# Optimization experiments

Hardware: AMD Instinct MI355X
Metric: run time of the kernel (lower is better)

Reference implementation:

```python
import jax, jax.numpy as jnp
import numpy as np

N_WINDOW = 5
FEATS = 512
N_HIDDEN = 16
N = N_WINDOW * FEATS  # 2560


def leaky(x, slope):
    return jnp.where(x >= 0, x, slope * x)


def setup_inputs() -> dict:
    key = jax.random.key(0)
    ks = jax.random.split(key, 16)
    s = 0.05
    return {
        "data": jax.random.normal(ks[0], (1, N_WINDOW, FEATS), jnp.float32),
        "W1": jax.random.normal(ks[1], (N_HIDDEN, N), jnp.float32) * s,
        "b1": jax.random.normal(ks[2], (N_HIDDEN,), jnp.float32) * s,
        "W2": jax.random.normal(ks[3], (N_HIDDEN, N_HIDDEN), jnp.float32) * s,
        "b2": jax.random.normal(ks[4], (N_HIDDEN,), jnp.float32) * s,
        "W3": jax.random.normal(ks[5], (N_WINDOW, N_HIDDEN), jnp.float32) * s,
        "b3": jax.random.normal(ks[6], (N_WINDOW,), jnp.float32) * s,
        "gat_w": jax.random.normal(ks[7], (FEATS,), jnp.float32) * s,
        "a_src": jax.random.normal(ks[8], (FEATS,), jnp.float32) * s,
        "a_dst": jax.random.normal(ks[9], (FEATS,), jnp.float32) * s,
        "gat_bias": jax.random.normal(ks[10], (FEATS,), jnp.float32) * s,
        "F1": jax.random.normal(ks[11], (N_HIDDEN, FEATS), jnp.float32) * s,
        "fb1": jax.random.normal(ks[12], (N_HIDDEN,), jnp.float32) * s,
        "F2": jax.random.normal(ks[13], (N_WINDOW, N_HIDDEN), jnp.float32) * s,
        "fb2": jax.random.normal(ks[14], (N_WINDOW,), jnp.float32) * s,
    }


def reference(data, W1, b1, W2, b2, W3, b3, gat_w, a_src, a_dst, gat_bias, F1, fb1, F2, fb2):
    # ---- attention MLP: Flatten -> Linear -> LeakyReLU(1.0) -> Linear -> LeakyReLU(1.0) -> Linear -> Softmax(dim=0)
    flat = data.reshape(data.shape[0], -1)          # (1, n)
    h = leaky(flat @ W1.T + b1, 1.0)                 # slope True==1.0 -> identity (faithful)
    h = leaky(h @ W2.T + b2, 1.0)
    scores = h @ W3.T + b3                           # (1, n_window)
    att = jax.nn.softmax(scores, axis=0)             # softmax over batch dim (size 1 -> ones)
    att = att.reshape(-1, N_WINDOW, 1)               # (1, 5, 1)

    # ---- weighted window reduction: data_r = data^T @ att
    d = data.reshape(-1, N_WINDOW, FEATS)            # (1, 5, feats)
    data_r = jnp.matmul(jnp.swapaxes(d, -1, -2), att)  # (1, feats, 1)
    x = data_r.reshape(FEATS)                        # node features, scalar per node

    # ---- GATConv(in=1, out=1, heads=feats) on complete graph (self loops included)
    xW = x[:, None] * gat_w[None, :]                 # (N, H): per-head linear transform
    e_src = xW * a_src[None, :]                      # (N, H)
    e_dst = xW * a_dst[None, :]                      # (N, H)
    # logits e[i, j, h] for dst i, src j, head h
    e = leaky(e_dst[:, None, :] + e_src[None, :, :], 0.2)   # (N, N, H)
    alpha = jax.nn.softmax(e, axis=1)                # softmax over source nodes j
    feat_r = jnp.einsum('ijh,jh->ih', alpha, xW) + gat_bias  # (feats, feats)

    # ---- fcn: Linear -> LeakyReLU(1.0) -> Linear -> Sigmoid
    y = leaky(feat_r @ F1.T + fb1, 1.0)
    y = jax.nn.sigmoid(y @ F2.T + fb2)               # (feats, 5)
    return y.reshape(-1)
```

## Files before the change

kernel.cpp:

```cpp
#include <hip/hip_runtime.h>
#include <hip/hip_bf16.h>

#define FEATS 512
#define NW 5
#define NH 16
#define NOUT 5

#define MOFF 1024
#define GOFF (MOFF + 8 * 513)
#define COFF (GOFF + NOUT * FEATS)
#define WS_FLOATS_NEEDED (COFF + NOUT)

template <int CTRL, int RMASK>
__device__ __forceinline__ float dpp_addf(float v) {
    const int r = __builtin_amdgcn_update_dpp(0, __float_as_int(v), CTRL, RMASK, 0xf, true);
    return v + __int_as_float(r);
}
__device__ __forceinline__ float scan64(float v) {
    v = dpp_addf<0x111, 0xf>(v);
    v = dpp_addf<0x112, 0xf>(v);
    v = dpp_addf<0x114, 0xf>(v);
    v = dpp_addf<0x118, 0xf>(v);
    v = dpp_addf<0x142, 0xa>(v);
    v = dpp_addf<0x143, 0xc>(v);
    return v;
}
template <int CTRL, int RMASK>
__device__ __forceinline__ int dpp_addi(int v) {
    const int r = __builtin_amdgcn_update_dpp(0, v, CTRL, RMASK, 0xf, true);
    return v + r;
}
__device__ __forceinline__ int scan64i(int v) {
    v = dpp_addi<0x111, 0xf>(v);
    v = dpp_addi<0x112, 0xf>(v);
    v = dpp_addi<0x114, 0xf>(v);
    v = dpp_addi<0x118, 0xf>(v);
    v = dpp_addi<0x142, 0xa>(v);
    v = dpp_addi<0x143, 0xc>(v);
    return v;
}

__global__ __launch_bounds__(512) void prep_sort(const float* __restrict__ data,
                                                 float* __restrict__ ws) {
    __shared__ float xs[FEATS];
    const int t = threadIdx.x;
    float v = 0.f;
    #pragma unroll
    for (int w = 0; w < NW; ++w) v += data[w * FEATS + t];
    xs[t] = v;
    __syncthreads();

    const int wid = t >> 6, lane = t & 63;
    const int i = blockIdx.x * 8 + wid;
    const float vi = xs[i];
    int r = 0;
    #pragma unroll
    for (int u = 0; u < 8; ++u) {
        const int j = u * 64 + lane;
        const float xj = xs[j];
        r += (xj < vi) || (xj == vi && j < i);
    }
    r = scan64i(r);
    if (lane == 63) ws[FEATS + r] = vi;
    if (blockIdx.x == 0) ws[t] = xs[t];
}

__global__ __launch_bounds__(512) void moments(const float* __restrict__ F1,
                                               const float* __restrict__ fb1,
                                               const float* __restrict__ F2,
                                               const float* __restrict__ fb2,
                                               float* __restrict__ ws) {
    __shared__ float wt[8][8];
    const int t = threadIdx.x, lane = t & 63, wid = t >> 6;

    const float u = ws[FEATS + t];
    const float u2 = u * u,  u3 = u2 * u, u4 = u3 * u;
    const float u5 = u4 * u, u6 = u5 * u, u7 = u6 * u, u8 = u7 * u;

    float s1 = scan64(u),  s2 = scan64(u2), s3 = scan64(u3), s4 = scan64(u4);
    float s5 = scan64(u5), s6 = scan64(u6), s7 = scan64(u7), s8 = scan64(u8);
    if (lane == 63) {
        wt[0][wid] = s1; wt[1][wid] = s2; wt[2][wid] = s3; wt[3][wid] = s4;
        wt[4][wid] = s5; wt[5][wid] = s6; wt[6][wid] = s7; wt[7][wid] = s8;
    }
    __syncthreads();
    float o1 = 0, o2 = 0, o3 = 0, o4 = 0, o5 = 0, o6 = 0, o7 = 0, o8 = 0;
    #pragma unroll
    for (int w = 0; w < 7; ++w) {
        if (w < wid) {
            o1 += wt[0][w]; o2 += wt[1][w]; o3 += wt[2][w]; o4 += wt[3][w];
            o5 += wt[4][w]; o6 += wt[5][w]; o7 += wt[6][w]; o8 += wt[7][w];
        }
    }
    ws[MOFF + 0 * 513 + t + 1] = s1 + o1;  ws[MOFF + 1 * 513 + t + 1] = s2 + o2;
    ws[MOFF + 2 * 513 + t + 1] = s3 + o3;  ws[MOFF + 3 * 513 + t + 1] = s4 + o4;
    ws[MOFF + 4 * 513 + t + 1] = s5 + o5;  ws[MOFF + 5 * 513 + t + 1] = s6 + o6;
    ws[MOFF + 6 * 513 + t + 1] = s7 + o7;  ws[MOFF + 7 * 513 + t + 1] = s8 + o8;
    if (t == 0) {
        #pragma unroll
        for (int p = 0; p < 8; ++p) ws[MOFF + p * 513] = 0.f;
    }

    #pragma unroll
    for (int o = 0; o < NOUT; ++o) {
        float g = 0.f;
        #pragma unroll
        for (int k = 0; k < NH; ++k) g = fmaf(F2[o * NH + k], F1[k * FEATS + t], g);
        ws[GOFF + o * FEATS + t] = g;
    }
    if (t < NOUT) {
        float c = fb2[t];
        #pragma unroll
        for (int k = 0; k < NH; ++k) c = fmaf(F2[t * NH + k], fb1[k], c);
        ws[COFF + t] = c;
    }
}

__global__ __launch_bounds__(512) void gat_out(
    const float* __restrict__ ws,
    const float* __restrict__ gat_w, const float* __restrict__ a_src,
    const float* __restrict__ a_dst, const float* __restrict__ gat_bias,
    float* __restrict__ out)
{
    __shared__ float xsrt[FEATS];
    __shared__ float Mt[8 * 513];
    __shared__ float part[NOUT][8];

    const int t = threadIdx.x, lane = t & 63, wid = t >> 6;
    const int i = blockIdx.x;
    const float LOG2E = 1.4426950408889634f;

    xsrt[t] = ws[FEATS + t];
    #pragma unroll
    for (int q = 0; q < 8; ++q) Mt[q * 512 + t] = ws[MOFF + q * 512 + t];
    if (t < 8) Mt[4096 + t] = ws[MOFF + 4096 + t];

    const float xi   = ws[i];
    const float gw   = gat_w[t];
    const float asr  = a_src[t];
    const float ads  = a_dst[t];
    const float bias = gat_bias[t];
    float Gv[NOUT];
    #pragma unroll
    for (int o = 0; o < NOUT; ++o) Gv[o] = ws[GOFF + o * FEATS + t];
    __syncthreads();

    const float a  = gw * asr;
    const float d  = gw * ads * xi;
    const float a2 = 0.2f * a;
    const bool csn = (a >= 0.f);

    int m = 0;
    #pragma unroll
    for (int step = 256; step; step >>= 1) {
        const int cand = m + step;
        const float tt = fmaf(xsrt[cand - 1], a, d);
        const bool p = csn ? (tt >= 0.f) : (tt < 0.f);
        if (!p) m = cand;
    }

    float P[8], N[8];
    #pragma unroll
    for (int p = 0; p < 8; ++p) {
        const float Pp = Mt[p * 513 + m];
        const float Tp = Mt[p * 513 + 512];
        P[p] = Pp; N[p] = Tp - Pp;
    }
    const float P0 = (float)m, N0 = (float)(FEATS - m);

    float Fv_[8], Qv_[8];
    #pragma unroll
    for (int p = 0; p < 8; ++p) { Fv_[p] = csn ? N[p] : P[p]; Qv_[p] = csn ? P[p] : N[p]; }
    const float F0 = csn ? N0 : P0;
    const float Q0 = csn ? P0 : N0;

    const float r2 = 0.5f, r3 = 1.f/6.f, r4 = 1.f/24.f, r5 = 1.f/120.f,
                r6 = 1.f/720.f, r7 = 1.f/5040.f;
    float h;
    h = Fv_[6] * r7; h = fmaf(h, a, Fv_[5] * r6); h = fmaf(h, a, Fv_[4] * r5);
    h = fmaf(h, a, Fv_[3] * r4); h = fmaf(h, a, Fv_[2] * r3); h = fmaf(h, a, Fv_[1] * r2);
    h = fmaf(h, a, Fv_[0]);
    const float Fe = fmaf(h, a, F0);
    h = Fv_[7] * r7; h = fmaf(h, a, Fv_[6] * r6); h = fmaf(h, a, Fv_[5] * r5);
    h = fmaf(h, a, Fv_[4] * r4); h = fmaf(h, a, Fv_[3] * r3); h = fmaf(h, a, Fv_[2] * r2);
    h = fmaf(h, a, Fv_[1]);
    const float Fw = fmaf(h, a, Fv_[0]);
    h = Qv_[6] * r7; h = fmaf(h, a2, Qv_[5] * r6); h = fmaf(h, a2, Qv_[4] * r5);
    h = fmaf(h, a2, Qv_[3] * r4); h = fmaf(h, a2, Qv_[2] * r3); h = fmaf(h, a2, Qv_[1] * r2);
    h = fmaf(h, a2, Qv_[0]);
    const float Pe = fmaf(h, a2, Q0);
    h = Qv_[7] * r7; h = fmaf(h, a2, Qv_[6] * r6); h = fmaf(h, a2, Qv_[5] * r5);
    h = fmaf(h, a2, Qv_[4] * r4); h = fmaf(h, a2, Qv_[3] * r3); h = fmaf(h, a2, Qv_[2] * r2);
    h = fmaf(h, a2, Qv_[1]);
    const float Pw = fmaf(h, a2, Qv_[0]);

    const float A1 = __builtin_amdgcn_exp2f(LOG2E * d);
    const float A2 = __builtin_amdgcn_exp2f(0.2f * LOG2E * d);
    const float Se = A1 * Fe + A2 * Pe;
    const float Sv = A1 * Fw + A2 * Pw;
    const float feat = gw * (Sv / Se) + bias;

    #pragma unroll
    for (int o = 0; o < NOUT; ++o) {
        const float p = scan64(feat * Gv[o]);
        if (lane == 63) part[o][wid] = p;
    }
    __syncthreads();
    if (t < NOUT) {
        float s = ws[COFF + t];
        #pragma unroll
        for (int w = 0; w < 8; ++w) s += part[t][w];
        out[i * NOUT + t] = 1.f / (1.f + __builtin_amdgcn_exp2f(-s * LOG2E));
    }
}

__global__ __launch_bounds__(512) void gat_fused_fb(
    const float* __restrict__ data,
    const float* __restrict__ gat_w, const float* __restrict__ a_src,
    const float* __restrict__ a_dst, const float* __restrict__ gat_bias,
    const float* __restrict__ F1, const float* __restrict__ fb1,
    const float* __restrict__ F2, const float* __restrict__ fb2,
    float* __restrict__ out)
{
    __shared__ __align__(16) float xs[FEATS];
    __shared__ float feat[FEATS];
    __shared__ float part[NH][8];
    __shared__ float hv[NH];
    const int h = threadIdx.x;
    const int i = blockIdx.x;
    float v = 0.f;
    #pragma unroll
    for (int w = 0; w < NW; ++w) v += data[w * FEATS + h];
    xs[h] = v;
    __syncthreads();
    const float LOG2E = 1.4426950408889634f;
    const float gwv = gat_w[h];
    const float cs = gwv * a_src[h] * LOG2E;
    const float cd = gwv * a_dst[h] * LOG2E;
    const float di = xs[i] * cd;
    float se = 0.f, sv = 0.f;
    const float4* x4 = (const float4*)xs;
    for (int j4 = 0; j4 < FEATS / 4; ++j4) {
        float4 q = x4[j4];
        #pragma unroll
        for (int u = 0; u < 4; ++u) {
            float xj = (u == 0) ? q.x : (u == 1) ? q.y : (u == 2) ? q.z : q.w;
            float tt = fmaf(xj, cs, di);
            float l  = fmaxf(tt, 0.2f * tt);
            float e  = __builtin_amdgcn_exp2f(l);
            se += e;
            sv = fmaf(e, xj, sv);
        }
    }
    feat[h] = gwv * sv / se + gat_bias[h];
    __syncthreads();
    const int lane = h & 63, wid = h >> 6;
    const float fv = feat[h];
    for (int k = 0; k < NH; ++k) {
        float p = fv * F1[k * FEATS + h];
        #pragma unroll
        for (int off = 32; off; off >>= 1) p += __shfl_xor(p, off);
        if (lane == 0) part[k][wid] = p;
    }
    __syncthreads();
    if (h < NH) {
        float s = fb1[h];
        #pragma unroll
        for (int w = 0; w < 8; ++w) s += part[h][w];
        hv[h] = s;
    }
    __syncthreads();
    if (h < 5) {
        float s = fb2[h];
        #pragma unroll
        for (int k = 0; k < NH; ++k) s = fmaf(hv[k], F2[h * NH + k], s);
        out[i * 5 + h] = 1.f / (1.f + __builtin_amdgcn_exp2f(-s * LOG2E));
    }
}

extern "C" void kernel_launch(void* const* d_in, const int* in_sizes, int n_in,
                              void* d_out, int out_size, void* d_ws, size_t ws_size,
                              hipStream_t stream) {
    (void)in_sizes; (void)n_in; (void)out_size;
    const float* data     = (const float*)d_in[0];
    const float* gat_w    = (const float*)d_in[7];
    const float* a_src    = (const float*)d_in[8];
    const float* a_dst    = (const float*)d_in[9];
    const float* gat_bias = (const float*)d_in[10];
    const float* F1       = (const float*)d_in[11];
    const float* fb1      = (const float*)d_in[12];
    const float* F2       = (const float*)d_in[13];
    const float* fb2      = (const float*)d_in[14];
    float* out = (float*)d_out;

    if (ws_size >= (size_t)WS_FLOATS_NEEDED * sizeof(float)) {
        float* ws = (float*)d_ws;
        prep_sort<<<64, FEATS, 0, stream>>>(data, ws);
        moments<<<1, FEATS, 0, stream>>>(F1, fb1, F2, fb2, ws);
        gat_out<<<FEATS, FEATS, 0, stream>>>(ws, gat_w, a_src, a_dst, gat_bias, out);
    } else {
        gat_fused_fb<<<FEATS, FEATS, 0, stream>>>(data, gat_w, a_src, a_dst, gat_bias,
                                                  F1, fb1, F2, fb2, out);
    }
}
```

Baseline: 17.52 us.

## Fuse moments kernel into GAT output kernel, recomputing prefix moments per block

Removes the single-block moments kernel and folds its work into the per-row GAT kernel. Each of the 512 blocks now recomputes the power prefix sums of the sorted features, the F2·F1 projection and the bias constant itself, and reads x_i directly from the input data. This drops one kernel launch and a serial single-block stage plus the workspace round trip, in exchange for redundant per-block computation and extra global reads of F1.

```diff
diff --git a/kernel.cpp b/kernel.cpp
--- a/kernel.cpp
+++ b/kernel.cpp
@@ -6,10 +6,7 @@
 #define NH 16
 #define NOUT 5
 
-#define MOFF 1024
-#define GOFF (MOFF + 8 * 513)
-#define COFF (GOFF + NOUT * FEATS)
-#define WS_FLOATS_NEEDED (COFF + NOUT)
+#define WS_FLOATS_NEEDED FEATS
 
 template <int CTRL, int RMASK>
 __device__ __forceinline__ float dpp_addf(float v) {
@@ -61,28 +58,54 @@
         r += (xj < vi) || (xj == vi && j < i);
     }
     r = scan64i(r);
-    if (lane == 63) ws[FEATS + r] = vi;
-    if (blockIdx.x == 0) ws[t] = xs[t];
-}
-
-__global__ __launch_bounds__(512) void moments(const float* __restrict__ F1,
-                                               const float* __restrict__ fb1,
-                                               const float* __restrict__ F2,
-                                               const float* __restrict__ fb2,
-                                               float* __restrict__ ws) {
+    if (lane == 63) ws[r] = vi;
+}
+
+__global__ __launch_bounds__(512) void gat_all(
+    const float* __restrict__ ws, const float* __restrict__ data,
+    const float* __restrict__ gat_w, const float* __restrict__ a_src,
+    const float* __restrict__ a_dst, const float* __restrict__ gat_bias,
+    const float* __restrict__ F1, const float* __restrict__ fb1,
+    const float* __restrict__ F2, const float* __restrict__ fb2,
+    float* __restrict__ out)
+{
+    __shared__ float xsrt[FEATS];
+    __shared__ float Mt[8 * 513];
     __shared__ float wt[8][8];
+    __shared__ float part[NOUT][8];
+
     const int t = threadIdx.x, lane = t & 63, wid = t >> 6;
-
-    const float u = ws[FEATS + t];
+    const int i = blockIdx.x;
+    const float LOG2E = 1.4426950408889634f;
+
+    const float u = ws[t];
+    xsrt[t] = u;
+
     const float u2 = u * u,  u3 = u2 * u, u4 = u3 * u;
     const float u5 = u4 * u, u6 = u5 * u, u7 = u6 * u, u8 = u7 * u;
-
     float s1 = scan64(u),  s2 = scan64(u2), s3 = scan64(u3), s4 = scan64(u4);
     float s5 = scan64(u5), s6 = scan64(u6), s7 = scan64(u7), s8 = scan64(u8);
     if (lane == 63) {
         wt[0][wid] = s1; wt[1][wid] = s2; wt[2][wid] = s3; wt[3][wid] = s4;
         wt[4][wid] = s5; wt[5][wid] = s6; wt[6][wid] = s7; wt[7][wid] = s8;
     }
+
+    const float gw   = gat_w[t];
+    const float asr  = a_src[t];
+    const float ads  = a_dst[t];
+    const float bias = gat_bias[t];
+    float Gv[NOUT];
+    #pragma unroll
+    for (int o = 0; o < NOUT; ++o) {
+        float g = 0.f;
+        #pragma unroll
+        for (int k = 0; k < NH; ++k) g = fmaf(F2[o * NH + k], F1[k * FEATS + t], g);
+        Gv[o] = g;
+    }
+    float xi = 0.f;
+    #pragma unroll
+    for (int w = 0; w < NW; ++w) xi += data[w * FEATS + i];
+
     __syncthreads();
     float o1 = 0, o2 = 0, o3 = 0, o4 = 0, o5 = 0, o6 = 0, o7 = 0, o8 = 0;
     #pragma unroll
@@ -92,57 +115,14 @@
             o5 += wt[4][w]; o6 += wt[5][w]; o7 += wt[6][w]; o8 += wt[7][w];
         }
     }
-    ws[MOFF + 0 * 513 + t + 1] = s1 + o1;  ws[MOFF + 1 * 513 + t + 1] = s2 + o2;
-    ws[MOFF + 2 * 513 + t + 1] = s3 + o3;  ws[MOFF + 3 * 513 + t + 1] = s4 + o4;
-    ws[MOFF + 4 * 513 + t + 1] = s5 + o5;  ws[MOFF + 5 * 513 + t + 1] = s6 + o6;
-    ws[MOFF + 6 * 513 + t + 1] = s7 + o7;  ws[MOFF + 7 * 513 + t + 1] = s8 + o8;
+    Mt[0 * 513 + t + 1] = s1 + o1;  Mt[1 * 513 + t + 1] = s2 + o2;
+    Mt[2 * 513 + t + 1] = s3 + o3;  Mt[3 * 513 + t + 1] = s4 + o4;
+    Mt[4 * 513 + t + 1] = s5 + o5;  Mt[5 * 513 + t + 1] = s6 + o6;
+    Mt[6 * 513 + t + 1] = s7 + o7;  Mt[7 * 513 + t + 1] = s8 + o8;
     if (t == 0) {
         #pragma unroll
-        for (int p = 0; p < 8; ++p) ws[MOFF + p * 513] = 0.f;
-    }
-
-    #pragma unroll
-    for (int o = 0; o < NOUT; ++o) {
-        float g = 0.f;
-        #pragma unroll
-        for (int k = 0; k < NH; ++k) g = fmaf(F2[o * NH + k], F1[k * FEATS + t], g);
-        ws[GOFF + o * FEATS + t] = g;
-    }
-    if (t < NOUT) {
-        float c = fb2[t];
-        #pragma unroll
-        for (int k = 0; k < NH; ++k) c = fmaf(F2[t * NH + k], fb1[k], c);
-        ws[COFF + t] = c;
-    }
-}
-
-__global__ __launch_bounds__(512) void gat_out(
-    const float* __restrict__ ws,
-    const float* __restrict__ gat_w, const float* __restrict__ a_src,
-    const float* __restrict__ a_dst, const float* __restrict__ gat_bias,
-    float* __restrict__ out)
-{
-    __shared__ float xsrt[FEATS];
-    __shared__ float Mt[8 * 513];
-    __shared__ float part[NOUT][8];
-
-    const int t = threadIdx.x, lane = t & 63, wid = t >> 6;
-    const int i = blockIdx.x;
-    const float LOG2E = 1.4426950408889634f;
-
-    xsrt[t] = ws[FEATS + t];
-    #pragma unroll
-    for (int q = 0; q < 8; ++q) Mt[q * 512 + t] = ws[MOFF + q * 512 + t];
-    if (t < 8) Mt[4096 + t] = ws[MOFF + 4096 + t];
-
-    const float xi   = ws[i];
-    const float gw   = gat_w[t];
-    const float asr  = a_src[t];
-    const float ads  = a_dst[t];
-    const float bias = gat_bias[t];
-    float Gv[NOUT];
-    #pragma unroll
-    for (int o = 0; o < NOUT; ++o) Gv[o] = ws[GOFF + o * FEATS + t];
+        for (int p = 0; p < 8; ++p) Mt[p * 513] = 0.f;
+    }
     __syncthreads();
 
     const float a  = gw * asr;
@@ -207,7 +187,9 @@
     }
     __syncthreads();
     if (t < NOUT) {
-        float s = ws[COFF + t];
+        float s = fb2[t];
+        #pragma unroll
+        for (int k = 0; k < NH; ++k) s = fmaf(F2[t * NH + k], fb1[k], s);
         #pragma unroll
         for (int w = 0; w < 8; ++w) s += part[t][w];
         out[i * NOUT + t] = 1.f / (1.f + __builtin_amdgcn_exp2f(-s * LOG2E));
@@ -243,8 +225,8 @@
     for (int j4 = 0; j4 < FEATS / 4; ++j4) {
         float4 q = x4[j4];
         #pragma unroll
-        for (int u = 0; u < 4; ++u) {
-            float xj = (u == 0) ? q.x : (u == 1) ? q.y : (u == 2) ? q.z : q.w;
+        for (int uu = 0; uu < 4; ++uu) {
+            float xj = (uu == 0) ? q.x : (uu == 1) ? q.y : (uu == 2) ? q.z : q.w;
             float tt = fmaf(xj, cs, di);
             float l  = fmaxf(tt, 0.2f * tt);
             float e  = __builtin_amdgcn_exp2f(l);
@@ -296,8 +278,8 @@
     if (ws_size >= (size_t)WS_FLOATS_NEEDED * sizeof(float)) {
         float* ws = (float*)d_ws;
         prep_sort<<<64, FEATS, 0, stream>>>(data, ws);
-        moments<<<1, FEATS, 0, stream>>>(F1, fb1, F2, fb2, ws);
-        gat_out<<<FEATS, FEATS, 0, stream>>>(ws, gat_w, a_src, a_dst, gat_bias, out);
+        gat_all<<<FEATS, FEATS, 0, stream>>>(ws, data, gat_w, a_src, a_dst, gat_bias,
+                                             F1, fb1, F2, fb2, out);
     } else {
         gat_fused_fb<<<FEATS, FEATS, 0, stream>>>(data, gat_w, a_src, a_dst, gat_bias,
                                                   F1, fb1, F2, fb2, out);
```

Measured after the change: 15.53 us. 11.3% less time.
